# Kernel optimization log

Hardware: AMD Instinct MI355X
Metric: run time of the kernel (lower is better)

## Reference

```python
import jax, jax.numpy as jnp
import numpy as np

BATCH, SEQ, D_IN, D_ST = 16, 8192, 64, 128  # in_features=64, out_features(state)=128


def setup_inputs() -> dict:
    key = jax.random.key(0)
    k0, k1, k2, k3 = jax.random.split(key, 4)
    x = jax.random.normal(k0, (BATCH, SEQ, D_IN), dtype=jnp.float32)
    # State-transition matrix A (HiPPO-initialized in the original). We draw a
    # random dense matrix scaled to spectral radius ~0.9 so the 8192-step
    # recurrence stays numerically stable.
    A = jax.random.normal(k1, (D_ST, D_ST), dtype=jnp.float32) * (0.9 / np.sqrt(D_ST))
    Bw = jax.random.normal(k2, (D_ST, D_IN), dtype=jnp.float32) / np.sqrt(D_IN)
    Bb = jnp.zeros((D_ST,), dtype=jnp.float32)  # bias=True on B
    Cw = jax.random.normal(k3, (D_IN, D_ST), dtype=jnp.float32) / np.sqrt(D_ST)
    return {"x": x, "A": A, "Bw": Bw, "Bb": Bb, "Cw": Cw}


def reference(x, A, Bw, Bb, Cw):
    # Discrete linear SSM: h_t = A h_{t-1} + (B x_t + b),  y_t = C h_t
    # Input projection is batched into one big GEMM (not per-step).
    bx = jnp.einsum('bsi,di->bsd', x, Bw) + Bb          # [B,S,D_ST]
    bx_t = jnp.transpose(bx, (1, 0, 2))                  # [S,B,D_ST]

    def step(h, u):
        h = u + h @ A.T                                  # [B,D_ST]
        return h, h

    h0 = jnp.zeros((x.shape[0], A.shape[0]), dtype=x.dtype)
    _, hs = jax.lax.scan(step, h0, bx_t)                 # hs: [S,B,D_ST]
    # Output projection as one big GEMM after the scan.
    y = jnp.einsum('sbd,od->bso', hs, Cw)                # [B,S,D_IN]
    return y
```

## Files before the change

kernel.cpp:

```cpp
#include <hip/hip_runtime.h>


#define SEQ   8192
#define DIN   64
#define LCH   16
#define NCH   (SEQ / LCH)
#define KCOMB 7

typedef _Float16 v8h __attribute__((ext_vector_type(8)));
typedef __fp16   v2h __attribute__((ext_vector_type(2)));
typedef float    v4f __attribute__((ext_vector_type(4)));

#define MFMA(a, b, c) __builtin_amdgcn_mfma_f32_16x16x32_f16((a), (b), (c), 0, 0, 0)
#define PKRTZ __builtin_amdgcn_cvt_pkrtz
#define Z4 (v4f{0.f, 0.f, 0.f, 0.f})

#define OFF_AH 0
#define OFF_AL 16384
#define OFF_BH 32768
#define OFF_BL 40960
#define OFF_CH 49152
#define OFF_CL 57344
#define OFF_TH 65536
#define OFF_TL 81920

__device__ __forceinline__ void block_sync() {
  asm volatile("s_waitcnt lgkmcnt(0)" ::: "memory");
  __builtin_amdgcn_s_barrier();
  asm volatile("" ::: "memory");
}

__device__ __forceinline__ int rho_fwd(int lidx) {
  int kt = lidx >> 5, q = (lidx >> 3) & 3, e = lidx & 7;
  int eh = e >> 1;
  int m = kt + 4 * (eh & 1);
  int r = 2 * (eh >> 1) + (e & 1);
  return 16 * m + 4 * q + r;
}
__device__ __forceinline__ int rho_inv(int p) {
  int m = p >> 4, q = (p >> 2) & 3, r = p & 3;
  int eh = ((r >> 1) << 1) | (m >> 2);
  int e  = (eh << 1) | (r & 1);
  return 32 * (m & 3) + 8 * q + e;
}
__device__ __forceinline__ void pack_hl(float v, _Float16* hp, _Float16* lp) {
  _Float16 h = (_Float16)v;
  *hp = h; *lp = (_Float16)(v - (float)h);
}

__global__ void mmk(const float* __restrict__ X, const float* __restrict__ Y,
                    float* __restrict__ D) {
  int idx = blockIdx.x * 256 + threadIdx.x;
  int i = idx >> 7, j = idx & 127;
  const float* xr = X + i * 128;
  const float* yc = Y + j;
  float s0 = 0.f, s1 = 0.f, s2 = 0.f, s3 = 0.f;
#pragma unroll
  for (int k = 0; k < 128; k += 4) {
    s0 = fmaf(xr[k],     yc[(k)     * 128], s0);
    s1 = fmaf(xr[k + 1], yc[(k + 1) * 128], s1);
    s2 = fmaf(xr[k + 2], yc[(k + 2) * 128], s2);
    s3 = fmaf(xr[k + 3], yc[(k + 3) * 128], s3);
  }
  D[idx] = (s0 + s1) + (s2 + s3);
}

__global__ void packk(const float* __restrict__ A, const float* __restrict__ Bw,
                      const float* __restrict__ Bb, const float* __restrict__ Cw,
                      const float* __restrict__ A8, _Float16* __restrict__ F,
                      float* __restrict__ Bbs) {
  int idx = blockIdx.x * 256 + threadIdx.x;
  if (idx < 16384) {
    int i = idx >> 7, j = idx & 127;
    int o = rho_fwd(i) * 128 + j;
    pack_hl(A[idx], F + OFF_AH + o, F + OFF_AL + o);
  } else if (idx < 24576) {
    int p = idx - 16384; int i = p >> 6, j = p & 63;
    int o = rho_fwd(i) * 64 + j;
    pack_hl(Bw[p], F + OFF_BH + o, F + OFF_BL + o);
  } else if (idx < 32768) {
    int p = idx - 24576;
    pack_hl(Cw[p], F + OFF_CH + p, F + OFF_CL + p);
  } else if (idx < 32896) {
    int i = idx - 32768;
    Bbs[i] = Bb[rho_inv(i)];
  } else if (idx < 49280) {
    int p = idx - 32896; int i = p >> 7, j = p & 127;
    const float* xr = A8 + i * 128;
    const float* yc = A8 + j;
    float s0 = 0.f, s1 = 0.f, s2 = 0.f, s3 = 0.f;
#pragma unroll
    for (int k = 0; k < 128; k += 4) {
      s0 = fmaf(xr[k],     yc[(k)     * 128], s0);
      s1 = fmaf(xr[k + 1], yc[(k + 1) * 128], s1);
      s2 = fmaf(xr[k + 2], yc[(k + 2) * 128], s2);
      s3 = fmaf(xr[k + 3], yc[(k + 3) * 128], s3);
    }
    float v = (s0 + s1) + (s2 + s3);
    int o = rho_fwd(i) * 128 + j;
    pack_hl(v, F + OFF_TH + o, F + OFF_TL + o);
  }
}

__device__ __forceinline__ void split16(const v4f* b, v8h& xh0, v8h& xh1,
                                        v8h& xl0, v8h& xl1) {
  union { v2h h2[4]; v8h h8; } H0, H1;
  H0.h2[0] = PKRTZ(b[0][0], b[0][1]); H0.h2[1] = PKRTZ(b[0][2], b[0][3]);
  H0.h2[2] = PKRTZ(b[1][0], b[1][1]); H0.h2[3] = PKRTZ(b[1][2], b[1][3]);
  H1.h2[0] = PKRTZ(b[2][0], b[2][1]); H1.h2[1] = PKRTZ(b[2][2], b[2][3]);
  H1.h2[2] = PKRTZ(b[3][0], b[3][1]); H1.h2[3] = PKRTZ(b[3][2], b[3][3]);
  float r[16];
#pragma unroll
  for (int i = 0; i < 8; ++i) r[i]     = b[i >> 2][i & 3]       - (float)H0.h8[i];
#pragma unroll
  for (int i = 0; i < 8; ++i) r[8 + i] = b[2 + (i >> 2)][i & 3] - (float)H1.h8[i];
  union { v2h h2[4]; v8h h8; } L0, L1;
  L0.h2[0] = PKRTZ(r[0], r[1]);   L0.h2[1] = PKRTZ(r[2], r[3]);
  L0.h2[2] = PKRTZ(r[4], r[5]);   L0.h2[3] = PKRTZ(r[6], r[7]);
  L1.h2[0] = PKRTZ(r[8], r[9]);   L1.h2[1] = PKRTZ(r[10], r[11]);
  L1.h2[2] = PKRTZ(r[12], r[13]); L1.h2[3] = PKRTZ(r[14], r[15]);
  xh0 = H0.h8; xh1 = H1.h8; xl0 = L0.h8; xl1 = L1.h8;
}

__global__ __launch_bounds__(256, 2) void scan1(
    const float* __restrict__ x, const _Float16* __restrict__ F,
    const float* __restrict__ Bbs, float* __restrict__ Vbuf) {
  const int tid = threadIdx.x;
  const int wv  = tid >> 6;
  const int l   = tid & 63;
  const int n   = l & 15;
  const int q   = l >> 4;
  const int c   = blockIdx.x;
  const int t0  = c * LCH;

  v8h afh[2][4], afl[2][4], bwh[2][2], bwl[2][2];
  v4f bb2[2];
#pragma unroll
  for (int i = 0; i < 2; ++i) {
    int row = 16 * (wv + 4 * i) + n;
#pragma unroll
    for (int kt = 0; kt < 4; ++kt) {
      afh[i][kt] = *(const v8h*)(F + OFF_AH + row * 128 + 32 * kt + 8 * q);
      afl[i][kt] = *(const v8h*)(F + OFF_AL + row * 128 + 32 * kt + 8 * q);
    }
#pragma unroll
    for (int k2 = 0; k2 < 2; ++k2) {
      bwh[i][k2] = *(const v8h*)(F + OFF_BH + row * 64 + 32 * k2 + 8 * q);
      bwl[i][k2] = *(const v8h*)(F + OFF_BL + row * 64 + 32 * k2 + 8 * q);
    }
    bb2[i] = *(const v4f*)(Bbs + 16 * (wv + 4 * i) + 4 * q);
  }

  __shared__ _Float16 hx[2][2][4][512];

  const float* xb = x + (size_t)n * (SEQ * DIN) + 8 * q;
  v4f bufA[4], bufB[4], uA[2], uB[2];
  auto loadx = [&](v4f(&buf)[4], int t) {
    const float* p = xb + (size_t)t * DIN;
    buf[0] = *(const v4f*)(p);      buf[1] = *(const v4f*)(p + 4);
    buf[2] = *(const v4f*)(p + 32); buf[3] = *(const v4f*)(p + 36);
  };
  auto build_u = [&](const v4f(&b)[4]) {
    v8h xh0, xh1, xl0, xl1;
    split16(b, xh0, xh1, xl0, xl1);
#pragma unroll
    for (int i = 0; i < 2; ++i) {
      v4f a = bb2[i];
      a = MFMA(bwh[i][0], xh0, a);
      a = MFMA(bwh[i][1], xh1, a);
      uA[i] = a;
      v4f b1 = MFMA(bwl[i][0], xh0, Z4);
      b1 = MFMA(bwl[i][1], xh1, b1);
      v4f b2 = MFMA(bwh[i][0], xl0, Z4);
      b2 = MFMA(bwh[i][1], xl1, b2);
      uB[i] = b1 + b2;
    }
  };
  auto xwrite = [&](int pr, const v4f& a0, const v4f& a1) {
    union { v2h h2[4]; v8h h8; } U;
    U.h2[0] = PKRTZ(a0[0], a0[1]); U.h2[1] = PKRTZ(a1[0], a1[1]);
    U.h2[2] = PKRTZ(a0[2], a0[3]); U.h2[3] = PKRTZ(a1[2], a1[3]);
    *(v8h*)&hx[pr][0][wv][l * 8] = U.h8;
    float r0 = a0[0] - (float)U.h8[0], r1 = a0[1] - (float)U.h8[1];
    float r2 = a1[0] - (float)U.h8[2], r3 = a1[1] - (float)U.h8[3];
    float r4 = a0[2] - (float)U.h8[4], r5 = a0[3] - (float)U.h8[5];
    float r6 = a1[2] - (float)U.h8[6], r7 = a1[3] - (float)U.h8[7];
    union { v2h h2[4]; v8h h8; } L;
    L.h2[0] = PKRTZ(r0, r1); L.h2[1] = PKRTZ(r2, r3);
    L.h2[2] = PKRTZ(r4, r5); L.h2[3] = PKRTZ(r6, r7);
    *(v8h*)&hx[pr][1][wv][l * 8] = L.h8;
  };

  v8h hf[4], hlo[4];
#pragma unroll
  for (int kt = 0; kt < 4; ++kt) { hf[kt] = v8h{}; hlo[kt] = v8h{}; }

  auto rec24 = [&](v4f(&acc)[2]) {
#pragma unroll
    for (int i = 0; i < 2; ++i) {
      v4f a = MFMA(afh[i][0], hf[0], uA[i]);
      a     = MFMA(afh[i][1], hf[1], a);
      v4f b = MFMA(afh[i][2], hf[2], Z4);
      b     = MFMA(afh[i][3], hf[3], b);
      v4f c2a = MFMA(afl[i][0], hf[0], uB[i]);
      c2a     = MFMA(afl[i][1], hf[1], c2a);
      v4f c2b = MFMA(afl[i][2], hf[2], Z4);
      c2b     = MFMA(afl[i][3], hf[3], c2b);
      v4f c3a = MFMA(afh[i][0], hlo[0], Z4);
      c3a     = MFMA(afh[i][1], hlo[1], c3a);
      v4f c3b = MFMA(afh[i][2], hlo[2], Z4);
      c3b     = MFMA(afh[i][3], hlo[3], c3b);
      acc[i] = (a + b) + (c2a + c2b) + (c3a + c3b);
    }
  };

  auto step = [&](int t, v4f(&bsrc)[4], v4f(&bld)[4], int pr) {
    int tn = t + 2; if (tn > SEQ - 1) tn = SEQ - 1;
    loadx(bld, tn);
    v4f acc[2];
    rec24(acc);
    xwrite(pr, acc[0], acc[1]);
    block_sync();
    build_u(bsrc);
#pragma unroll
    for (int kt = 0; kt < 4; ++kt) {
      hf[kt]  = *(const v8h*)&hx[pr][0][kt][l * 8];
      hlo[kt] = *(const v8h*)&hx[pr][1][kt][l * 8];
    }
  };

  loadx(bufA, t0);
  loadx(bufB, t0 + 1);
  build_u(bufA);
#pragma unroll
  for (int tp = 0; tp < 7; ++tp) {
    step(t0 + 2 * tp,     bufB, bufA, 0);
    step(t0 + 2 * tp + 1, bufA, bufB, 1);
  }
  step(t0 + 14, bufB, bufA, 0);
  v4f acc[2];
  rec24(acc);
  float* vb = Vbuf + (size_t)c * 2048 + tid * 8;
  *(v4f*)vb       = acc[0];
  *(v4f*)(vb + 4) = acc[1];
}

__global__ __launch_bounds__(256, 2) void scan2(
    const float* __restrict__ x, float* __restrict__ y,
    const _Float16* __restrict__ F, const float* __restrict__ Bbs,
    const float* __restrict__ Vbuf) {
  const int tid = threadIdx.x;
  const int wv  = tid >> 6;
  const int l   = tid & 63;
  const int n   = l & 15;
  const int q   = l >> 4;
  const int c   = blockIdx.x;
  const int t0  = c * LCH, te = t0 + LCH;

  __shared__ _Float16 hx[2][2][4][512];

  const float* xb = x + (size_t)n * (SEQ * DIN) + 8 * q;
  float* yb = y + (size_t)n * (SEQ * DIN);
  v4f bufA[4], bufB[4];
  auto loadx = [&](v4f(&buf)[4], int t) {
    const float* p = xb + (size_t)t * DIN;
    buf[0] = *(const v4f*)(p);      buf[1] = *(const v4f*)(p + 4);
    buf[2] = *(const v4f*)(p + 32); buf[3] = *(const v4f*)(p + 36);
  };
  loadx(bufA, t0);
  loadx(bufB, t0 + 1);

  v8h afh[2][4], afl[2][4];
  auto load_AF = [&](int oh, int ol) {
#pragma unroll
    for (int i = 0; i < 2; ++i) {
      int row = 16 * (wv + 4 * i) + n;
#pragma unroll
      for (int kt = 0; kt < 4; ++kt) {
        afh[i][kt] = *(const v8h*)(F + oh + row * 128 + 32 * kt + 8 * q);
        afl[i][kt] = *(const v8h*)(F + ol + row * 128 + 32 * kt + 8 * q);
      }
    }
  };

  auto xwrite = [&](int pr, const v4f& a0, const v4f& a1) {
    union { v2h h2[4]; v8h h8; } U;
    U.h2[0] = PKRTZ(a0[0], a0[1]); U.h2[1] = PKRTZ(a1[0], a1[1]);
    U.h2[2] = PKRTZ(a0[2], a0[3]); U.h2[3] = PKRTZ(a1[2], a1[3]);
    *(v8h*)&hx[pr][0][wv][l * 8] = U.h8;
    float r0 = a0[0] - (float)U.h8[0], r1 = a0[1] - (float)U.h8[1];
    float r2 = a1[0] - (float)U.h8[2], r3 = a1[1] - (float)U.h8[3];
    float r4 = a0[2] - (float)U.h8[4], r5 = a0[3] - (float)U.h8[5];
    float r6 = a1[2] - (float)U.h8[6], r7 = a1[3] - (float)U.h8[7];
    union { v2h h2[4]; v8h h8; } L;
    L.h2[0] = PKRTZ(r0, r1); L.h2[1] = PKRTZ(r2, r3);
    L.h2[2] = PKRTZ(r4, r5); L.h2[3] = PKRTZ(r6, r7);
    *(v8h*)&hx[pr][1][wv][l * 8] = L.h8;
  };

  v8h hf[4], hlo[4];
#pragma unroll
  for (int kt = 0; kt < 4; ++kt) { hf[kt] = v8h{}; hlo[kt] = v8h{}; }

  int pr = 0;

  if (c > 0) {
    load_AF(OFF_TH, OFF_TL);
    const int kmax = (c < KCOMB) ? c : KCOMB;
    const float* vp = Vbuf + (size_t)(c - kmax) * 2048 + tid * 8;
    v4f v0 = *(const v4f*)vp, v1 = *(const v4f*)(vp + 4);
    for (int kk = kmax; kk >= 1; --kk) {
      v4f vc0 = v0, vc1 = v1;
      if (kk > 1) {
        const float* vn = Vbuf + (size_t)(c - kk + 1) * 2048 + tid * 8;
        v0 = *(const v4f*)vn; v1 = *(const v4f*)(vn + 4);
      }
      v4f acc[2];
#pragma unroll
      for (int i = 0; i < 2; ++i) {
        v4f ui = (i == 0) ? vc0 : vc1;
        v4f a = MFMA(afh[i][0], hf[0], ui);
        a     = MFMA(afh[i][1], hf[1], a);
        v4f b = MFMA(afh[i][2], hf[2], Z4);
        b     = MFMA(afh[i][3], hf[3], b);
        v4f c2a = MFMA(afl[i][0], hf[0], Z4);
        c2a     = MFMA(afl[i][1], hf[1], c2a);
        v4f c2b = MFMA(afl[i][2], hf[2], Z4);
        c2b     = MFMA(afl[i][3], hf[3], c2b);
        v4f c3a = MFMA(afh[i][0], hlo[0], Z4);
        c3a     = MFMA(afh[i][1], hlo[1], c3a);
        v4f c3b = MFMA(afh[i][2], hlo[2], Z4);
        c3b     = MFMA(afh[i][3], hlo[3], c3b);
        acc[i] = (a + b) + (c2a + c2b) + (c3a + c3b);
      }
      xwrite(pr, acc[0], acc[1]);
      block_sync();
#pragma unroll
      for (int kt = 0; kt < 4; ++kt) {
        hf[kt]  = *(const v8h*)&hx[pr][0][kt][l * 8];
        hlo[kt] = *(const v8h*)&hx[pr][1][kt][l * 8];
      }
      pr ^= 1;
    }
  }
  load_AF(OFF_AH, OFF_AL);

  v8h bwh[2][2], bwl[2][2], cwh[4], cwl[4];
  v4f bb2[2];
#pragma unroll
  for (int i = 0; i < 2; ++i) {
    int row = 16 * (wv + 4 * i) + n;
#pragma unroll
    for (int k2 = 0; k2 < 2; ++k2) {
      bwh[i][k2] = *(const v8h*)(F + OFF_BH + row * 64 + 32 * k2 + 8 * q);
      bwl[i][k2] = *(const v8h*)(F + OFF_BL + row * 64 + 32 * k2 + 8 * q);
    }
    bb2[i] = *(const v4f*)(Bbs + 16 * (wv + 4 * i) + 4 * q);
  }
  {
    int row = 16 * wv + n;
#pragma unroll
    for (int kt = 0; kt < 4; ++kt) {
      cwh[kt] = *(const v8h*)(F + OFF_CH + row * 128 + 32 * kt + 8 * q);
      cwl[kt] = *(const v8h*)(F + OFF_CL + row * 128 + 32 * kt + 8 * q);
    }
  }

  v4f uA[2], uB[2];
  auto build_u = [&](const v4f(&b)[4]) {
    v8h xh0, xh1, xl0, xl1;
    split16(b, xh0, xh1, xl0, xl1);
#pragma unroll
    for (int i = 0; i < 2; ++i) {
      v4f a = bb2[i];
      a = MFMA(bwh[i][0], xh0, a);
      a = MFMA(bwh[i][1], xh1, a);
      uA[i] = a;
      v4f b1 = MFMA(bwl[i][0], xh0, Z4);
      b1 = MFMA(bwl[i][1], xh1, b1);
      v4f b2 = MFMA(bwh[i][0], xl0, Z4);
      b2 = MFMA(bwh[i][1], xl1, b2);
      uB[i] = b1 + b2;
    }
  };
  auto emit_y = [&](int t) {
    v4f e1a = MFMA(cwh[1], hf[1], MFMA(cwh[0], hf[0], Z4));
    v4f e1b = MFMA(cwh[3], hf[3], MFMA(cwh[2], hf[2], Z4));
    v4f e2a = MFMA(cwh[1], hlo[1], MFMA(cwh[0], hlo[0], Z4));
    v4f e2b = MFMA(cwh[3], hlo[3], MFMA(cwh[2], hlo[2], Z4));
    v4f e3a = MFMA(cwl[1], hf[1], MFMA(cwl[0], hf[0], Z4));
    v4f e3b = MFMA(cwl[3], hf[3], MFMA(cwl[2], hf[2], Z4));
    v4f r = (e1a + e1b) + (e2a + e2b) + (e3a + e3b);
    *(v4f*)(yb + (size_t)t * DIN + 16 * wv + 4 * q) = r;
  };
  auto stepE = [&](int t, v4f(&bsrc)[4], v4f(&bld)[4], bool emit) {
    int tn = t + 2; if (tn > SEQ - 1) tn = SEQ - 1;
    loadx(bld, tn);
    if (emit) emit_y(t - 1);
    v4f acc[2];
#pragma unroll
    for (int i = 0; i < 2; ++i) {
      v4f a = MFMA(afh[i][0], hf[0], uA[i]);
      a     = MFMA(afh[i][1], hf[1], a);
      v4f b = MFMA(afh[i][2], hf[2], Z4);
      b     = MFMA(afh[i][3], hf[3], b);
      v4f c2a = MFMA(afl[i][0], hf[0], uB[i]);
      c2a     = MFMA(afl[i][1], hf[1], c2a);
      v4f c2b = MFMA(afl[i][2], hf[2], Z4);
      c2b     = MFMA(afl[i][3], hf[3], c2b);
      v4f c3a = MFMA(afh[i][0], hlo[0], Z4);
      c3a     = MFMA(afh[i][1], hlo[1], c3a);
      v4f c3b = MFMA(afh[i][2], hlo[2], Z4);
      c3b     = MFMA(afh[i][3], hlo[3], c3b);
      acc[i] = (a + b) + (c2a + c2b) + (c3a + c3b);
    }
    xwrite(pr, acc[0], acc[1]);
    block_sync();
    build_u(bsrc);
#pragma unroll
    for (int kt = 0; kt < 4; ++kt) {
      hf[kt]  = *(const v8h*)&hx[pr][0][kt][l * 8];
      hlo[kt] = *(const v8h*)&hx[pr][1][kt][l * 8];
    }
    pr ^= 1;
  };

  build_u(bufA);
#pragma unroll
  for (int tp = 0; tp < 8; ++tp) {
    stepE(t0 + 2 * tp,     bufB, bufA, tp > 0);
    stepE(t0 + 2 * tp + 1, bufA, bufB, true);
  }
  emit_y(te - 1);
}

extern "C" void kernel_launch(void* const* d_in, const int* in_sizes, int n_in,
                              void* d_out, int out_size, void* d_ws, size_t ws_size,
                              hipStream_t stream) {
  const float* x  = (const float*)d_in[0];
  const float* A  = (const float*)d_in[1];
  const float* Bw = (const float*)d_in[2];
  const float* Bb = (const float*)d_in[3];
  const float* Cw = (const float*)d_in[4];
  float* y = (float*)d_out;

  _Float16* F    = (_Float16*)d_ws;
  float*    Bbs  = (float*)((char*)d_ws + 196608);
  float*    pw   = (float*)((char*)d_ws + 197120);
  float*    Vbuf = (float*)((char*)d_ws + 393728);

  float* A2 = pw;
  float* A4 = pw + 16384;
  float* A8 = pw + 32768;

  mmk<<<64, 256, 0, stream>>>(A,  A,  A2);
  mmk<<<64, 256, 0, stream>>>(A2, A2, A4);
  mmk<<<64, 256, 0, stream>>>(A4, A4, A8);
  packk<<<193, 256, 0, stream>>>(A, Bw, Bb, Cw, A8, F, Bbs);
  scan1<<<NCH, 256, 0, stream>>>(x, F, Bbs, Vbuf);
  scan2<<<NCH, 256, 0, stream>>>(x, y, F, Bbs, Vbuf);
}
```

Before: 90.66 us.

## Process two independent chunks per block to interleave recurrence chains

Each block in scan1 and scan2 now handles two sequence chunks and interleaves their serial MFMA recurrence chains, so one barrier serves both chunks and latency is hidden by instruction-level parallelism. The grid is halved and launch bounds drop to one block per CU to make room for the doubled register state. In scan2 the carry-combination loop now always runs KCOMB iterations with zero fill for early chunks, which adds some redundant work for the first blocks. Register pressure and reduced occupancy could offset the gain.

```diff
diff --git a/kernel.cpp b/kernel.cpp
--- a/kernel.cpp
+++ b/kernel.cpp
@@ -122,7 +122,7 @@
   xh0 = H0.h8; xh1 = H1.h8; xl0 = L0.h8; xl1 = L1.h8;
 }
 
-__global__ __launch_bounds__(256, 2) void scan1(
+__global__ __launch_bounds__(256, 1) void scan1(
     const float* __restrict__ x, const _Float16* __restrict__ F,
     const float* __restrict__ Bbs, float* __restrict__ Vbuf) {
   const int tid = threadIdx.x;
@@ -130,8 +130,7 @@
   const int l   = tid & 63;
   const int n   = l & 15;
   const int q   = l >> 4;
-  const int c   = blockIdx.x;
-  const int t0  = c * LCH;
+  const int c0  = blockIdx.x * 2;
 
   v8h afh[2][4], afl[2][4], bwh[2][2], bwl[2][2];
   v4f bb2[2];
@@ -151,16 +150,22 @@
     bb2[i] = *(const v4f*)(Bbs + 16 * (wv + 4 * i) + 4 * q);
   }
 
-  __shared__ _Float16 hx[2][2][4][512];
+  __shared__ _Float16 hx[2][2][2][4][512];
 
   const float* xb = x + (size_t)n * (SEQ * DIN) + 8 * q;
-  v4f bufA[4], bufB[4], uA[2], uB[2];
+  v4f bufA[2][4], bufB[2][4], uA[2][2], uB[2][2];
+  v8h hf[2][4], hlo[2][4];
+#pragma unroll
+  for (int ch = 0; ch < 2; ++ch)
+#pragma unroll
+    for (int kt = 0; kt < 4; ++kt) { hf[ch][kt] = v8h{}; hlo[ch][kt] = v8h{}; }
+
   auto loadx = [&](v4f(&buf)[4], int t) {
     const float* p = xb + (size_t)t * DIN;
     buf[0] = *(const v4f*)(p);      buf[1] = *(const v4f*)(p + 4);
     buf[2] = *(const v4f*)(p + 32); buf[3] = *(const v4f*)(p + 36);
   };
-  auto build_u = [&](const v4f(&b)[4]) {
+  auto build_u = [&](int ch, const v4f(&b)[4]) {
     v8h xh0, xh1, xl0, xl1;
     split16(b, xh0, xh1, xl0, xl1);
 #pragma unroll
@@ -168,19 +173,19 @@
       v4f a = bb2[i];
       a = MFMA(bwh[i][0], xh0, a);
       a = MFMA(bwh[i][1], xh1, a);
-      uA[i] = a;
+      uA[ch][i] = a;
       v4f b1 = MFMA(bwl[i][0], xh0, Z4);
       b1 = MFMA(bwl[i][1], xh1, b1);
       v4f b2 = MFMA(bwh[i][0], xl0, Z4);
       b2 = MFMA(bwh[i][1], xl1, b2);
-      uB[i] = b1 + b2;
-    }
-  };
-  auto xwrite = [&](int pr, const v4f& a0, const v4f& a1) {
+      uB[ch][i] = b1 + b2;
+    }
+  };
+  auto xwrite = [&](int ch, int pr, const v4f& a0, const v4f& a1) {
     union { v2h h2[4]; v8h h8; } U;
     U.h2[0] = PKRTZ(a0[0], a0[1]); U.h2[1] = PKRTZ(a1[0], a1[1]);
     U.h2[2] = PKRTZ(a0[2], a0[3]); U.h2[3] = PKRTZ(a1[2], a1[3]);
-    *(v8h*)&hx[pr][0][wv][l * 8] = U.h8;
+    *(v8h*)&hx[ch][pr][0][wv][l * 8] = U.h8;
     float r0 = a0[0] - (float)U.h8[0], r1 = a0[1] - (float)U.h8[1];
     float r2 = a1[0] - (float)U.h8[2], r3 = a1[1] - (float)U.h8[3];
     float r4 = a0[2] - (float)U.h8[4], r5 = a0[3] - (float)U.h8[5];
@@ -188,64 +193,74 @@
     union { v2h h2[4]; v8h h8; } L;
     L.h2[0] = PKRTZ(r0, r1); L.h2[1] = PKRTZ(r2, r3);
     L.h2[2] = PKRTZ(r4, r5); L.h2[3] = PKRTZ(r6, r7);
-    *(v8h*)&hx[pr][1][wv][l * 8] = L.h8;
-  };
-
-  v8h hf[4], hlo[4];
-#pragma unroll
-  for (int kt = 0; kt < 4; ++kt) { hf[kt] = v8h{}; hlo[kt] = v8h{}; }
-
-  auto rec24 = [&](v4f(&acc)[2]) {
+    *(v8h*)&hx[ch][pr][1][wv][l * 8] = L.h8;
+  };
+  auto rec24 = [&](int ch, v4f(&acc)[2]) {
 #pragma unroll
     for (int i = 0; i < 2; ++i) {
-      v4f a = MFMA(afh[i][0], hf[0], uA[i]);
-      a     = MFMA(afh[i][1], hf[1], a);
-      v4f b = MFMA(afh[i][2], hf[2], Z4);
-      b     = MFMA(afh[i][3], hf[3], b);
-      v4f c2a = MFMA(afl[i][0], hf[0], uB[i]);
-      c2a     = MFMA(afl[i][1], hf[1], c2a);
-      v4f c2b = MFMA(afl[i][2], hf[2], Z4);
-      c2b     = MFMA(afl[i][3], hf[3], c2b);
-      v4f c3a = MFMA(afh[i][0], hlo[0], Z4);
-      c3a     = MFMA(afh[i][1], hlo[1], c3a);
-      v4f c3b = MFMA(afh[i][2], hlo[2], Z4);
-      c3b     = MFMA(afh[i][3], hlo[3], c3b);
+      v4f a = MFMA(afh[i][0], hf[ch][0], uA[ch][i]);
+      a     = MFMA(afh[i][1], hf[ch][1], a);
+      v4f b = MFMA(afh[i][2], hf[ch][2], Z4);
+      b     = MFMA(afh[i][3], hf[ch][3], b);
+      v4f c2a = MFMA(afl[i][0], hf[ch][0], uB[ch][i]);
+      c2a     = MFMA(afl[i][1], hf[ch][1], c2a);
+      v4f c2b = MFMA(afl[i][2], hf[ch][2], Z4);
+      c2b     = MFMA(afl[i][3], hf[ch][3], c2b);
+      v4f c3a = MFMA(afh[i][0], hlo[ch][0], Z4);
+      c3a     = MFMA(afh[i][1], hlo[ch][1], c3a);
+      v4f c3b = MFMA(afh[i][2], hlo[ch][2], Z4);
+      c3b     = MFMA(afh[i][3], hlo[ch][3], c3b);
       acc[i] = (a + b) + (c2a + c2b) + (c3a + c3b);
     }
   };
 
-  auto step = [&](int t, v4f(&bsrc)[4], v4f(&bld)[4], int pr) {
-    int tn = t + 2; if (tn > SEQ - 1) tn = SEQ - 1;
-    loadx(bld, tn);
+  auto step = [&](int trel, int po) {
+#pragma unroll
+    for (int ch = 0; ch < 2; ++ch) {
+      int tn = (c0 + ch) * LCH + trel + 2; if (tn > SEQ - 1) tn = SEQ - 1;
+      loadx(po ? bufB[ch] : bufA[ch], tn);
+    }
+    v4f acc[2][2];
+#pragma unroll
+    for (int ch = 0; ch < 2; ++ch) rec24(ch, acc[ch]);
+#pragma unroll
+    for (int ch = 0; ch < 2; ++ch) xwrite(ch, po, acc[ch][0], acc[ch][1]);
+    block_sync();
+#pragma unroll
+    for (int ch = 0; ch < 2; ++ch) build_u(ch, po ? bufA[ch] : bufB[ch]);
+#pragma unroll
+    for (int ch = 0; ch < 2; ++ch)
+#pragma unroll
+      for (int kt = 0; kt < 4; ++kt) {
+        hf[ch][kt]  = *(const v8h*)&hx[ch][po][0][kt][l * 8];
+        hlo[ch][kt] = *(const v8h*)&hx[ch][po][1][kt][l * 8];
+      }
+  };
+
+#pragma unroll
+  for (int ch = 0; ch < 2; ++ch) {
+    loadx(bufA[ch], (c0 + ch) * LCH);
+    loadx(bufB[ch], (c0 + ch) * LCH + 1);
+  }
+#pragma unroll
+  for (int ch = 0; ch < 2; ++ch) build_u(ch, bufA[ch]);
+#pragma unroll
+  for (int tp = 0; tp < 7; ++tp) {
+    step(2 * tp,     0);
+    step(2 * tp + 1, 1);
+  }
+  step(14, 0);
+#pragma unroll
+  for (int ch = 0; ch < 2; ++ch) {
     v4f acc[2];
-    rec24(acc);
-    xwrite(pr, acc[0], acc[1]);
-    block_sync();
-    build_u(bsrc);
-#pragma unroll
-    for (int kt = 0; kt < 4; ++kt) {
-      hf[kt]  = *(const v8h*)&hx[pr][0][kt][l * 8];
-      hlo[kt] = *(const v8h*)&hx[pr][1][kt][l * 8];
-    }
-  };
-
-  loadx(bufA, t0);
-  loadx(bufB, t0 + 1);
-  build_u(bufA);
-#pragma unroll
-  for (int tp = 0; tp < 7; ++tp) {
-    step(t0 + 2 * tp,     bufB, bufA, 0);
-    step(t0 + 2 * tp + 1, bufA, bufB, 1);
-  }
-  step(t0 + 14, bufB, bufA, 0);
-  v4f acc[2];
-  rec24(acc);
-  float* vb = Vbuf + (size_t)c * 2048 + tid * 8;
-  *(v4f*)vb       = acc[0];
-  *(v4f*)(vb + 4) = acc[1];
-}
-
-__global__ __launch_bounds__(256, 2) void scan2(
+    rec24(ch, acc);
+    float* vb = Vbuf + (size_t)(c0 + ch) * 2048 + tid * 8;
+    *(v4f*)vb       = acc[0];
+    *(v4f*)(vb + 4) = acc[1];
+  }
+}
+
+__global__ __launch_bounds__(256, 1) void scan2(
     const float* __restrict__ x, float* __restrict__ y,
     const _Float16* __restrict__ F, const float* __restrict__ Bbs,
     const float* __restrict__ Vbuf) {
@@ -254,21 +269,23 @@
   const int l   = tid & 63;
   const int n   = l & 15;
   const int q   = l >> 4;
-  const int c   = blockIdx.x;
-  const int t0  = c * LCH, te = t0 + LCH;
-
-  __shared__ _Float16 hx[2][2][4][512];
+  const int c0  = blockIdx.x * 2;
+
+  __shared__ _Float16 hx[2][2][2][4][512];
 
   const float* xb = x + (size_t)n * (SEQ * DIN) + 8 * q;
   float* yb = y + (size_t)n * (SEQ * DIN);
-  v4f bufA[4], bufB[4];
+  v4f bufA[2][4], bufB[2][4];
   auto loadx = [&](v4f(&buf)[4], int t) {
     const float* p = xb + (size_t)t * DIN;
     buf[0] = *(const v4f*)(p);      buf[1] = *(const v4f*)(p + 4);
     buf[2] = *(const v4f*)(p + 32); buf[3] = *(const v4f*)(p + 36);
   };
-  loadx(bufA, t0);
-  loadx(bufB, t0 + 1);
+#pragma unroll
+  for (int ch = 0; ch < 2; ++ch) {
+    loadx(bufA[ch], (c0 + ch) * LCH);
+    loadx(bufB[ch], (c0 + ch) * LCH + 1);
+  }
 
   v8h afh[2][4], afl[2][4];
   auto load_AF = [&](int oh, int ol) {
@@ -282,12 +299,11 @@
       }
     }
   };
-
-  auto xwrite = [&](int pr, const v4f& a0, const v4f& a1) {
+  auto xwrite = [&](int ch, int pr, const v4f& a0, const v4f& a1) {
     union { v2h h2[4]; v8h h8; } U;
     U.h2[0] = PKRTZ(a0[0], a0[1]); U.h2[1] = PKRTZ(a1[0], a1[1]);
     U.h2[2] = PKRTZ(a0[2], a0[3]); U.h2[3] = PKRTZ(a1[2], a1[3]);
-    *(v8h*)&hx[pr][0][wv][l * 8] = U.h8;
+    *(v8h*)&hx[ch][pr][0][wv][l * 8] = U.h8;
     float r0 = a0[0] - (float)U.h8[0], r1 = a0[1] - (float)U.h8[1];
     float r2 = a1[0] - (float)U.h8[2], r3 = a1[1] - (float)U.h8[3];
     float r4 = a0[2] - (float)U.h8[4], r5 = a0[3] - (float)U.h8[5];
@@ -295,56 +311,57 @@
     union { v2h h2[4]; v8h h8; } L;
     L.h2[0] = PKRTZ(r0, r1); L.h2[1] = PKRTZ(r2, r3);
     L.h2[2] = PKRTZ(r4, r5); L.h2[3] = PKRTZ(r6, r7);
-    *(v8h*)&hx[pr][1][wv][l * 8] = L.h8;
-  };
-
-  v8h hf[4], hlo[4];
-#pragma unroll
-  for (int kt = 0; kt < 4; ++kt) { hf[kt] = v8h{}; hlo[kt] = v8h{}; }
+    *(v8h*)&hx[ch][pr][1][wv][l * 8] = L.h8;
+  };
+
+  v8h hf[2][4], hlo[2][4];
+#pragma unroll
+  for (int ch = 0; ch < 2; ++ch)
+#pragma unroll
+    for (int kt = 0; kt < 4; ++kt) { hf[ch][kt] = v8h{}; hlo[ch][kt] = v8h{}; }
 
   int pr = 0;
 
-  if (c > 0) {
-    load_AF(OFF_TH, OFF_TL);
-    const int kmax = (c < KCOMB) ? c : KCOMB;
-    const float* vp = Vbuf + (size_t)(c - kmax) * 2048 + tid * 8;
-    v4f v0 = *(const v4f*)vp, v1 = *(const v4f*)(vp + 4);
-    for (int kk = kmax; kk >= 1; --kk) {
-      v4f vc0 = v0, vc1 = v1;
-      if (kk > 1) {
-        const float* vn = Vbuf + (size_t)(c - kk + 1) * 2048 + tid * 8;
-        v0 = *(const v4f*)vn; v1 = *(const v4f*)(vn + 4);
-      }
+  load_AF(OFF_TH, OFF_TL);
+  for (int kk = KCOMB; kk >= 1; --kk) {
+#pragma unroll
+    for (int ch = 0; ch < 2; ++ch) {
+      const int c = c0 + ch;
       v4f acc[2];
+      if (kk <= c) {
+        const float* vp = Vbuf + (size_t)(c - kk) * 2048 + tid * 8;
+        acc[0] = *(const v4f*)vp; acc[1] = *(const v4f*)(vp + 4);
+      } else { acc[0] = Z4; acc[1] = Z4; }
 #pragma unroll
       for (int i = 0; i < 2; ++i) {
-        v4f ui = (i == 0) ? vc0 : vc1;
-        v4f a = MFMA(afh[i][0], hf[0], ui);
-        a     = MFMA(afh[i][1], hf[1], a);
-        v4f b = MFMA(afh[i][2], hf[2], Z4);
-        b     = MFMA(afh[i][3], hf[3], b);
-        v4f c2a = MFMA(afl[i][0], hf[0], Z4);
-        c2a     = MFMA(afl[i][1], hf[1], c2a);
-        v4f c2b = MFMA(afl[i][2], hf[2], Z4);
-        c2b     = MFMA(afl[i][3], hf[3], c2b);
-        v4f c3a = MFMA(afh[i][0], hlo[0], Z4);
-        c3a     = MFMA(afh[i][1], hlo[1], c3a);
-        v4f c3b = MFMA(afh[i][2], hlo[2], Z4);
-        c3b     = MFMA(afh[i][3], hlo[3], c3b);
+        v4f a = MFMA(afh[i][0], hf[ch][0], acc[i]);
+        a     = MFMA(afh[i][1], hf[ch][1], a);
+        v4f b = MFMA(afh[i][2], hf[ch][2], Z4);
+        b     = MFMA(afh[i][3], hf[ch][3], b);
+        v4f c2a = MFMA(afl[i][0], hf[ch][0], Z4);
+        c2a     = MFMA(afl[i][1], hf[ch][1], c2a);
+        v4f c2b = MFMA(afl[i][2], hf[ch][2], Z4);
+        c2b     = MFMA(afl[i][3], hf[ch][3], c2b);
+        v4f c3a = MFMA(afh[i][0], hlo[ch][0], Z4);
+        c3a     = MFMA(afh[i][1], hlo[ch][1], c3a);
+        v4f c3b = MFMA(afh[i][2], hlo[ch][2], Z4);
+        c3b     = MFMA(afh[i][3], hlo[ch][3], c3b);
         acc[i] = (a + b) + (c2a + c2b) + (c3a + c3b);
       }
-      xwrite(pr, acc[0], acc[1]);
-      block_sync();
+      xwrite(ch, pr, acc[0], acc[1]);
+    }
+    block_sync();
+#pragma unroll
+    for (int ch = 0; ch < 2; ++ch)
 #pragma unroll
       for (int kt = 0; kt < 4; ++kt) {
-        hf[kt]  = *(const v8h*)&hx[pr][0][kt][l * 8];
-        hlo[kt] = *(const v8h*)&hx[pr][1][kt][l * 8];
-      }
-      pr ^= 1;
-    }
-  }
+        hf[ch][kt]  = *(const v8h*)&hx[ch][pr][0][kt][l * 8];
+        hlo[ch][kt] = *(const v8h*)&hx[ch][pr][1][kt][l * 8];
+      }
+    pr ^= 1;
+  }
+
   load_AF(OFF_AH, OFF_AL);
-
   v8h bwh[2][2], bwl[2][2], cwh[4], cwl[4];
   v4f bb2[2];
 #pragma unroll
@@ -366,8 +383,8 @@
     }
   }
 
-  v4f uA[2], uB[2];
-  auto build_u = [&](const v4f(&b)[4]) {
+  v4f uA[2][2], uB[2][2];
+  auto build_u = [&](int ch, const v4f(&b)[4]) {
     v8h xh0, xh1, xl0, xl1;
     split16(b, xh0, xh1, xl0, xl1);
 #pragma unroll
@@ -375,63 +392,78 @@
       v4f a = bb2[i];
       a = MFMA(bwh[i][0], xh0, a);
       a = MFMA(bwh[i][1], xh1, a);
-      uA[i] = a;
+      uA[ch][i] = a;
       v4f b1 = MFMA(bwl[i][0], xh0, Z4);
       b1 = MFMA(bwl[i][1], xh1, b1);
       v4f b2 = MFMA(bwh[i][0], xl0, Z4);
       b2 = MFMA(bwh[i][1], xl1, b2);
-      uB[i] = b1 + b2;
-    }
-  };
-  auto emit_y = [&](int t) {
-    v4f e1a = MFMA(cwh[1], hf[1], MFMA(cwh[0], hf[0], Z4));
-    v4f e1b = MFMA(cwh[3], hf[3], MFMA(cwh[2], hf[2], Z4));
-    v4f e2a = MFMA(cwh[1], hlo[1], MFMA(cwh[0], hlo[0], Z4));
-    v4f e2b = MFMA(cwh[3], hlo[3], MFMA(cwh[2], hlo[2], Z4));
-    v4f e3a = MFMA(cwl[1], hf[1], MFMA(cwl[0], hf[0], Z4));
-    v4f e3b = MFMA(cwl[3], hf[3], MFMA(cwl[2], hf[2], Z4));
+      uB[ch][i] = b1 + b2;
+    }
+  };
+  auto emit_y = [&](int ch, int t) {
+    v4f e1a = MFMA(cwh[1], hf[ch][1], MFMA(cwh[0], hf[ch][0], Z4));
+    v4f e1b = MFMA(cwh[3], hf[ch][3], MFMA(cwh[2], hf[ch][2], Z4));
+    v4f e2a = MFMA(cwh[1], hlo[ch][1], MFMA(cwh[0], hlo[ch][0], Z4));
+    v4f e2b = MFMA(cwh[3], hlo[ch][3], MFMA(cwh[2], hlo[ch][2], Z4));
+    v4f e3a = MFMA(cwl[1], hf[ch][1], MFMA(cwl[0], hf[ch][0], Z4));
+    v4f e3b = MFMA(cwl[3], hf[ch][3], MFMA(cwl[2], hf[ch][2], Z4));
     v4f r = (e1a + e1b) + (e2a + e2b) + (e3a + e3b);
     *(v4f*)(yb + (size_t)t * DIN + 16 * wv + 4 * q) = r;
   };
-  auto stepE = [&](int t, v4f(&bsrc)[4], v4f(&bld)[4], bool emit) {
-    int tn = t + 2; if (tn > SEQ - 1) tn = SEQ - 1;
-    loadx(bld, tn);
-    if (emit) emit_y(t - 1);
-    v4f acc[2];
-#pragma unroll
-    for (int i = 0; i < 2; ++i) {
-      v4f a = MFMA(afh[i][0], hf[0], uA[i]);
-      a     = MFMA(afh[i][1], hf[1], a);
-      v4f b = MFMA(afh[i][2], hf[2], Z4);
-      b     = MFMA(afh[i][3], hf[3], b);
-      v4f c2a = MFMA(afl[i][0], hf[0], uB[i]);
-      c2a     = MFMA(afl[i][1], hf[1], c2a);
-      v4f c2b = MFMA(afl[i][2], hf[2], Z4);
-      c2b     = MFMA(afl[i][3], hf[3], c2b);
-      v4f c3a = MFMA(afh[i][0], hlo[0], Z4);
-      c3a     = MFMA(afh[i][1], hlo[1], c3a);
-      v4f c3b = MFMA(afh[i][2], hlo[2], Z4);
-      c3b     = MFMA(afh[i][3], hlo[3], c3b);
-      acc[i] = (a + b) + (c2a + c2b) + (c3a + c3b);
-    }
-    xwrite(pr, acc[0], acc[1]);
+
+  auto stepE = [&](int trel, int po, bool em) {
+#pragma unroll
+    for (int ch = 0; ch < 2; ++ch) {
+      int tn = (c0 + ch) * LCH + trel + 2; if (tn > SEQ - 1) tn = SEQ - 1;
+      loadx(po ? bufB[ch] : bufA[ch], tn);
+    }
+    if (em) {
+#pragma unroll
+      for (int ch = 0; ch < 2; ++ch) emit_y(ch, (c0 + ch) * LCH + trel - 1);
+    }
+    v4f acc[2][2];
+#pragma unroll
+    for (int ch = 0; ch < 2; ++ch)
+#pragma unroll
+      for (int i = 0; i < 2; ++i) {
+        v4f a = MFMA(afh[i][0], hf[ch][0], uA[ch][i]);
+        a     = MFMA(afh[i][1], hf[ch][1], a);
+        v4f b = MFMA(afh[i][2], hf[ch][2], Z4);
+        b     = MFMA(afh[i][3], hf[ch][3], b);
+        v4f c2a = MFMA(afl[i][0], hf[ch][0], uB[ch][i]);
+        c2a     = MFMA(afl[i][1], hf[ch][1], c2a);
+        v4f c2b = MFMA(afl[i][2], hf[ch][2], Z4);
+        c2b     = MFMA(afl[i][3], hf[ch][3], c2b);
+        v4f c3a = MFMA(afh[i][0], hlo[ch][0], Z4);
+        c3a     = MFMA(afh[i][1], hlo[ch][1], c3a);
+        v4f c3b = MFMA(afh[i][2], hlo[ch][2], Z4);
+        c3b     = MFMA(afh[i][3], hlo[ch][3], c3b);
+        acc[ch][i] = (a + b) + (c2a + c2b) + (c3a + c3b);
+      }
+#pragma unroll
+    for (int ch = 0; ch < 2; ++ch) xwrite(ch, pr, acc[ch][0], acc[ch][1]);
     block_sync();
-    build_u(bsrc);
-#pragma unroll
-    for (int kt = 0; kt < 4; ++kt) {
-      hf[kt]  = *(const v8h*)&hx[pr][0][kt][l * 8];
-      hlo[kt] = *(const v8h*)&hx[pr][1][kt][l * 8];
-    }
+#pragma unroll
+    for (int ch = 0; ch < 2; ++ch) build_u(ch, po ? bufA[ch] : bufB[ch]);
+#pragma unroll
+    for (int ch = 0; ch < 2; ++ch)
+#pragma unroll
+      for (int kt = 0; kt < 4; ++kt) {
+        hf[ch][kt]  = *(const v8h*)&hx[ch][pr][0][kt][l * 8];
+        hlo[ch][kt] = *(const v8h*)&hx[ch][pr][1][kt][l * 8];
+      }
     pr ^= 1;
   };
 
-  build_u(bufA);
+#pragma unroll
+  for (int ch = 0; ch < 2; ++ch) build_u(ch, bufA[ch]);
 #pragma unroll
   for (int tp = 0; tp < 8; ++tp) {
-    stepE(t0 + 2 * tp,     bufB, bufA, tp > 0);
-    stepE(t0 + 2 * tp + 1, bufA, bufB, true);
-  }
-  emit_y(te - 1);
+    stepE(2 * tp,     0, tp > 0);
+    stepE(2 * tp + 1, 1, true);
+  }
+#pragma unroll
+  for (int ch = 0; ch < 2; ++ch) emit_y(ch, (c0 + ch) * LCH + LCH - 1);
 }
 
 extern "C" void kernel_launch(void* const* d_in, const int* in_sizes, int n_in,
@@ -457,6 +489,6 @@
   mmk<<<64, 256, 0, stream>>>(A2, A2, A4);
   mmk<<<64, 256, 0, stream>>>(A4, A4, A8);
   packk<<<193, 256, 0, stream>>>(A, Bw, Bb, Cw, A8, F, Bbs);
-  scan1<<<NCH, 256, 0, stream>>>(x, F, Bbs, Vbuf);
-  scan2<<<NCH, 256, 0, stream>>>(x, y, F, Bbs, Vbuf);
-}
+  scan1<<<NCH / 2, 256, 0, stream>>>(x, F, Bbs, Vbuf);
+  scan2<<<NCH / 2, 256, 0, stream>>>(x, y, F, Bbs, Vbuf);
+}
```

After: 103.9 us. 1.15x slower.
